# Performance work log

Hardware: AMD Instinct MI355X
Metric: run time of the kernel (lower is better)

## Reference

```python
import jax, jax.numpy as jnp
import numpy as np

N, E, B = 50000, 800000, 128
NF, ED, HID, HEADS, DH, OUT, L = 7, 2, 128, 4, 32, 64, 3
EPS = 1e-5
NEG_SLOPE = 0.2


def _layer_norm(x, g, b):
    mu = jnp.mean(x, axis=-1, keepdims=True)
    v = jnp.mean((x - mu) ** 2, axis=-1, keepdims=True)
    return g * (x - mu) / jnp.sqrt(v + EPS) + b


def setup_inputs() -> dict:
    key = jax.random.key(0)
    ks = jax.random.split(key, 32)
    s = 0.05
    inp = {
        "x": jax.random.normal(ks[0], (N, NF), jnp.float32),
        "edge_index": jax.random.randint(ks[1], (2, E), 0, N, jnp.int32),
        "edge_attr": jax.random.uniform(ks[2], (E, ED), jnp.float32),
        "batch": jnp.sort(jax.random.randint(ks[3], (N,), 0, B, jnp.int32)),
        # node encoder
        "enc_W": jax.random.normal(ks[4], (NF, HID)) * (1.0 / np.sqrt(NF)),
        "enc_b": jnp.zeros((HID,)),
        "enc_g": jnp.ones((HID,)),
        "enc_bb": jnp.zeros((HID,)),
        # GATv2 layers (stacked over L)
        "gat_Wsrc": jax.random.normal(ks[5], (L, HID, HID)) * (1.0 / np.sqrt(HID)),
        "gat_Wdst": jax.random.normal(ks[6], (L, HID, HID)) * (1.0 / np.sqrt(HID)),
        "gat_We": jax.random.normal(ks[7], (L, ED, HID)) * (1.0 / np.sqrt(ED)),
        "gat_att": jax.random.normal(ks[8], (L, HEADS, DH)) * s,
        "gat_bias": jnp.zeros((L, HID)),
        # GraphNorm per layer
        "gn_w": jnp.ones((L, HID)),
        "gn_b": jnp.zeros((L, HID)),
        "gn_s": jnp.ones((L, HID)),  # mean_scale
        # attention pooling
        "pool_W1": jax.random.normal(ks[9], (HID, HID)) * (1.0 / np.sqrt(HID)),
        "pool_b1": jnp.zeros((HID,)),
        "pool_W2": jax.random.normal(ks[10], (HID, 1)) * (1.0 / np.sqrt(HID)),
        # output mapper
        "map_W1": jax.random.normal(ks[11], (HID, HID)) * (1.0 / np.sqrt(HID)),
        "map_b1": jnp.zeros((HID,)),
        "map_g": jnp.ones((HID,)),
        "map_bb": jnp.zeros((HID,)),
        "map_W2": jax.random.normal(ks[12], (HID, OUT)) * (1.0 / np.sqrt(HID)),
        "map_b2": jnp.zeros((OUT,)),
    }
    return inp


def _segment_softmax(scores, seg, num_seg):
    # scores: [E2, HEADS], seg: [E2] destination node ids
    m = jax.ops.segment_max(scores, seg, num_segments=num_seg)
    ex = jnp.exp(scores - m[seg])
    denom = jax.ops.segment_sum(ex, seg, num_segments=num_seg)
    return ex / denom[seg]


def _gatv2(x, src, dst, ea, Wsrc, Wdst, We, att, bias):
    e2 = src.shape[0]
    xl = (x @ Wsrc)[src].reshape(e2, HEADS, DH)   # lin_l(x_j), source
    xr = (x @ Wdst)[dst].reshape(e2, HEADS, DH)   # lin_r(x_i), target
    ee = (ea @ We).reshape(e2, HEADS, DH)
    z = jax.nn.leaky_relu(xl + xr + ee, NEG_SLOPE)
    score = jnp.einsum("ehd,hd->eh", z, att)
    alpha = _segment_softmax(score, dst, N)       # softmax over incoming edges
    msg = (xl * alpha[:, :, None]).reshape(e2, HID)
    out = jax.ops.segment_sum(msg, dst, num_segments=N)
    return out + bias


def _graph_norm(x, batch, w, b, scale):
    cnt = jax.ops.segment_sum(jnp.ones((N,), x.dtype), batch, num_segments=B)
    cnt = jnp.maximum(cnt, 1.0)[:, None]
    mean = jax.ops.segment_sum(x, batch, num_segments=B) / cnt
    xc = x - scale * mean[batch]
    var = jax.ops.segment_sum(xc * xc, batch, num_segments=B) / cnt
    return w * xc / jnp.sqrt(var[batch] + EPS) + b


def reference(x, edge_index, edge_attr, batch, enc_W, enc_b, enc_g, enc_bb,
              gat_Wsrc, gat_Wdst, gat_We, gat_att, gat_bias, gn_w, gn_b, gn_s,
              pool_W1, pool_b1, pool_W2, map_W1, map_b1, map_g, map_bb,
              map_W2, map_b2):
    # node encoder: Linear -> ReLU -> LayerNorm
    h = _layer_norm(jax.nn.relu(x @ enc_W + enc_b), enc_g, enc_bb)

    # add self loops; self-loop edge_attr = mean of edge_attr (PyG fill_value='mean')
    loop = jnp.arange(N, dtype=edge_index.dtype)
    src = jnp.concatenate([edge_index[0], loop])
    dst = jnp.concatenate([edge_index[1], loop])
    ea_mean = jnp.mean(edge_attr, axis=0)
    ea = jnp.concatenate([edge_attr, jnp.broadcast_to(ea_mean, (N, ED))], axis=0)

    for i in range(L):
        out = _gatv2(h, src, dst, ea, gat_Wsrc[i], gat_Wdst[i], gat_We[i],
                     gat_att[i], gat_bias[i])
        out = out + h  # residual (in_dim == out_dim -> Identity proj)
        out = _graph_norm(out, batch, gn_w[i], gn_b[i], gn_s[i])
        h = jax.nn.elu(out)

    node_emb = h
    # attention pooling: softmax over ALL nodes (dim=0, as in source)
    scores = jnp.tanh(h @ pool_W1 + pool_b1) @ pool_W2          # [N, 1]
    weights = jax.nn.softmax(scores, axis=0)
    g = jax.ops.segment_sum(h * weights, batch, num_segments=B)  # [B, HID]

    # output mapper (dropout inactive at eval)
    g = _layer_norm(jax.nn.relu(g @ map_W1 + map_b1), map_g, map_bb)
    graph_emb = g @ map_W2 + map_b2
    return graph_emb, node_emb
```

## Files before the change

kernel.cpp:

```cpp
#include <hip/hip_runtime.h>
#include <hip/hip_bf16.h>

typedef __hip_bfloat16 bf16;
typedef __attribute__((ext_vector_type(8))) short short8;
typedef __attribute__((ext_vector_type(4))) float float4v;

#define Nn   50000
#define Ee   800000
#define E2   850000
#define Bb   128
#define NFd  7
#define HID  128
#define OUTD 64
#define EPS  1e-5f
#define SLOPE 0.2f
#define NSTRIP 3125
#define NPAIR  1563

#define MFMA16(a,b,c) __builtin_amdgcn_mfma_f32_16x16x32_bf16(a,b,c,0,0,0)

__device__ __forceinline__ float lane_bcast(float v, int l){
  return __int_as_float(__builtin_amdgcn_readlane(__float_as_int(v), l));
}
__device__ __forceinline__ float wred_sum(float v){
  #pragma unroll
  for (int o=32;o;o>>=1) v += __shfl_xor(v, o, 64);
  return v;
}
__device__ __forceinline__ float gred16_sum(float v){
  v += __shfl_xor(v,1,64); v += __shfl_xor(v,2,64);
  v += __shfl_xor(v,4,64); v += __shfl_xor(v,8,64);
  return v;
}
__device__ __forceinline__ unsigned fkey(float f){
  unsigned u = __float_as_uint(f);
  return (u & 0x80000000u) ? ~u : (u | 0x80000000u);
}
__device__ __forceinline__ float fkeyinv(unsigned k){
  unsigned u = (k & 0x80000000u) ? (k ^ 0x80000000u) : ~k;
  return __uint_as_float(u);
}
__device__ __forceinline__ float tanh_fast(float x){
  float e = __expf(fminf(fmaxf(2.f*x, -30.f), 30.f));
  return (e-1.f)/(e+1.f);
}
__device__ __forceinline__ float bf_lo(unsigned u){ return __uint_as_float(u<<16); }
__device__ __forceinline__ float bf_hi(unsigned u){ return __uint_as_float(u & 0xffff0000u); }
__device__ __forceinline__ unsigned short f2bs(float f){
  bf16 h = __float2bfloat16(f);
  return *reinterpret_cast<unsigned short*>(&h);
}
__device__ __forceinline__ unsigned pack2(float a, float b){
  return (unsigned)f2bs(a) | ((unsigned)f2bs(b) << 16);
}

__global__ __launch_bounds__(256) void k_encoder(
    const float* __restrict__ x, const float* __restrict__ W, const float* __restrict__ b,
    const float* __restrict__ g, const float* __restrict__ bbv,
    float* __restrict__ h, unsigned* __restrict__ hbu){
  int wv = (blockIdx.x*blockDim.x + threadIdx.x) >> 6;
  if (wv >= Nn) return;
  int lane = threadIdx.x & 63;
  int d0 = 2*lane, d1 = d0+1;
  float y0 = b[d0], y1 = b[d1];
  #pragma unroll
  for (int i=0;i<NFd;++i){
    float xv = x[wv*NFd + i];
    y0 = fmaf(xv, W[i*HID + d0], y0);
    y1 = fmaf(xv, W[i*HID + d1], y1);
  }
  y0 = fmaxf(y0, 0.f); y1 = fmaxf(y1, 0.f);
  float mu = wred_sum(y0+y1) * (1.f/HID);
  float c0 = y0-mu, c1 = y1-mu;
  float var = wred_sum(c0*c0 + c1*c1) * (1.f/HID);
  float rs = rsqrtf(var + EPS);
  float v0 = g[d0]*c0*rs + bbv[d0];
  float v1 = g[d1]*c1*rs + bbv[d1];
  *(float2*)(h + (size_t)wv*HID + d0) = make_float2(v0, v1);
  hbu[(size_t)wv*64 + lane] = pack2(v0, v1);
}

__global__ void k_ea_mean(const float* __restrict__ ea, float* __restrict__ eam){
  int tid = blockIdx.x*blockDim.x + threadIdx.x;
  const float2* ea2 = (const float2*)ea;
  float a0=0.f, a1=0.f;
  for (int e=tid; e<Ee; e += gridDim.x*blockDim.x){
    float2 v = ea2[e];
    a0 += v.x; a1 += v.y;
  }
  a0 = wred_sum(a0); a1 = wred_sum(a1);
  if ((threadIdx.x & 63)==0){
    atomicAdd(&eam[0], a0*(1.f/Ee));
    atomicAdd(&eam[1], a1*(1.f/Ee));
  }
}

__global__ void k_deg(const int* __restrict__ ei, int* __restrict__ deg){
  int e = blockIdx.x*blockDim.x + threadIdx.x;
  if (e >= E2) return;
  int d = (e < Ee) ? ei[Ee + e] : (e - Ee);
  atomicAdd(&deg[d], 1);
}

__global__ __launch_bounds__(1024) void k_scan(const int* __restrict__ deg,
    int* __restrict__ offs, int* __restrict__ cursor){
  __shared__ int wsum[16];
  __shared__ int tot_s;
  __shared__ int carry_s;
  int t = threadIdx.x, lane = t & 63, wid = t >> 6;
  if (t==0) carry_s = 0;
  __syncthreads();
  for (int base=0; base<Nn; base += 1024){
    int i = base + t;
    int v = (i < Nn) ? deg[i] : 0;
    int x = v;
    #pragma unroll
    for (int o=1;o<64;o<<=1){ int u = __shfl_up(x, o, 64); if (lane >= o) x += u; }
    if (lane==63) wsum[wid] = x;
    __syncthreads();
    if (t==0){ int s=0; for (int k=0;k<16;++k){ int tv=wsum[k]; wsum[k]=s; s+=tv; } tot_s = s; }
    __syncthreads();
    int excl = carry_s + wsum[wid] + x - v;
    if (i < Nn){ offs[i] = excl; cursor[i] = excl; }
    __syncthreads();
    if (t==0) carry_s += tot_s;
    __syncthreads();
  }
  if (t==0) offs[Nn] = carry_s;
}

__global__ void k_scatter(const int* __restrict__ ei, const float* __restrict__ ea,
    const float* __restrict__ eam, int* __restrict__ cursor,
    int* __restrict__ csrc, float2* __restrict__ cea){
  int e = blockIdx.x*blockDim.x + threadIdx.x;
  if (e >= E2) return;
  int s, d; float a0, a1;
  if (e < Ee){
    s = ei[e]; d = ei[Ee + e];
    float2 v = ((const float2*)ea)[e];
    a0 = v.x; a1 = v.y;
  } else {
    s = d = e - Ee; a0 = eam[0]; a1 = eam[1];
  }
  int pos = atomicAdd(&cursor[d], 1);
  csrc[pos] = s;
  cea[pos] = make_float2(a0, a1);
}

__global__ void k_gstart(const int* __restrict__ batch, int* __restrict__ gstart){
  int n = blockIdx.x*blockDim.x + threadIdx.x;
  if (n >= Nn) return;
  int bc = batch[n];
  int bp = (n==0) ? -1 : batch[n-1];
  for (int b = bp+1; b <= bc; ++b) gstart[b] = n;
  if (n == Nn-1){ for (int b = bc+1; b <= Bb; ++b) gstart[b] = Nn; }
}

__global__ __launch_bounds__(256) void k_dualgemm(
    const unsigned* __restrict__ hbu,
    const float* __restrict__ Wsrc, const float* __restrict__ Wdst,
    unsigned* __restrict__ hsb, float* __restrict__ hd){
  __shared__ unsigned short wt[256*HID];
  #pragma unroll
  for (int iter=0; iter<64; ++iter){
    int idx = iter*256 + threadIdx.x;
    int n = idx & 255, kp = idx >> 8;
    const float* Wp = (n < 128) ? Wsrc : (Wdst - 128);
    float w0 = Wp[(2*kp)*HID + n];
    float w1 = Wp[(2*kp+1)*HID + n];
    int byt = (n*256 + kp*4) ^ ((n&7)<<4);
    *(unsigned*)((char*)wt + byt) = pack2(w0, w1);
  }
  __syncthreads();
  int wid = threadIdx.x >> 6, lane = threadIdx.x & 63;
  int q = lane >> 4, c = lane & 15;
  const unsigned short* hb = (const unsigned short*)hbu;
  for (int pr = blockIdx.x*4 + wid; pr < NPAIR; pr += gridDim.x*4){
    int p0 = 2*pr, p1 = 2*pr + 1;
    bool v1 = (p1 < NSTRIP);
    int node0 = p0*16 + c;
    int node1 = v1 ? (p1*16 + c) : node0;
    short8 bf0[4], bf1[4];
    const unsigned short* hp0 = hb + (size_t)node0*HID + q*8;
    const unsigned short* hp1 = hb + (size_t)node1*HID + q*8;
    #pragma unroll
    for (int s=0;s<4;++s){
      bf0[s] = *(const short8*)(hp0 + s*32);
      bf1[s] = *(const short8*)(hp1 + s*32);
    }
    #pragma unroll 4
    for (int t=0;t<16;++t){
      float4v ac0 = {0.f,0.f,0.f,0.f}, ac1 = {0.f,0.f,0.f,0.f};
      #pragma unroll
      for (int s=0;s<4;++s){
        int row = t*16 + c;
        int byt = (row*256 + s*64 + q*16) ^ ((row&7)<<4);
        short8 af = *(const short8*)((const char*)wt + byt);
        ac0 = MFMA16(af, bf0[s], ac0);
        ac1 = MFMA16(af, bf1[s], ac1);
      }
      if (t < 8){
        int co = t*8 + q*2;
        *(uint2*)(hsb + (size_t)node0*64 + co) =
            make_uint2(pack2(ac0[0],ac0[1]), pack2(ac0[2],ac0[3]));
        if (v1) *(uint2*)(hsb + (size_t)node1*64 + co) =
            make_uint2(pack2(ac1[0],ac1[1]), pack2(ac1[2],ac1[3]));
      } else {
        int dd = (t-8)*16 + q*4;
        *(float4*)(hd + (size_t)node0*HID + dd) = make_float4(ac0[0],ac0[1],ac0[2],ac0[3]);
        if (v1) *(float4*)(hd + (size_t)node1*HID + dd) = make_float4(ac1[0],ac1[1],ac1[2],ac1[3]);
      }
    }
  }
}

__global__ __launch_bounds__(256) void k_edge(const unsigned* __restrict__ hsb,
    float* __restrict__ hdio, const float* __restrict__ h,
    const int* __restrict__ csrc, const float2* __restrict__ cea,
    const int* __restrict__ offs, const float* __restrict__ We,
    const float* __restrict__ att, const float* __restrict__ bias){
  int n = (blockIdx.x*blockDim.x + threadIdx.x) >> 6;
  if (n >= Nn) return;
  int lane = threadIdx.x & 63;
  int d0 = 2*lane, d1 = d0+1;
  float we00 = We[d0],       we01 = We[d1];
  float we10 = We[HID+d0],   we11 = We[HID+d1];
  float at0  = att[(lane>>4)*32 + (d0&31)];
  float at1  = att[(lane>>4)*32 + (d1&31)];
  float2 xr = *(const float2*)(hdio + (size_t)n*HID + d0);
  int e0 = offs[n], e1 = offs[n+1];
  float m = -1e30f, ssum = 0.f, acc0 = 0.f, acc1 = 0.f;
  int s_next = csrc[e0];
  float2 ea_next = cea[e0];
  for (int e = e0; e < e1; ++e){
    int s = s_next; float2 eav = ea_next;
    if (e+1 < e1){ s_next = csrc[e+1]; ea_next = cea[e+1]; }
    unsigned xlu = hsb[(size_t)s*64 + lane];
    float xl0 = bf_lo(xlu), xl1 = bf_hi(xlu);
    float z0 = fmaf(eav.y, we10, fmaf(eav.x, we00, xl0 + xr.x));
    float z1 = fmaf(eav.y, we11, fmaf(eav.x, we01, xl1 + xr.y));
    z0 = fmaxf(z0, SLOPE*z0);
    z1 = fmaxf(z1, SLOPE*z1);
    float sc = gred16_sum(fmaf(z1, at1, z0*at0));
    float nm = fmaxf(m, sc);
    float f  = __expf(m - nm);
    float p  = __expf(sc - nm);
    ssum = ssum*f + p;
    acc0 = fmaf(p, xl0, acc0*f);
    acc1 = fmaf(p, xl1, acc1*f);
    m = nm;
  }
  float inv = 1.f/ssum;
  float o0 = acc0*inv + bias[d0] + h[(size_t)n*HID + d0];
  float o1 = acc1*inv + bias[d1] + h[(size_t)n*HID + d1];
  *(float2*)(hdio + (size_t)n*HID + d0) = make_float2(o0, o1);
}

__global__ __launch_bounds__(128) void k_gn_reduce(const float* __restrict__ out,
    const int* __restrict__ gstart, float* __restrict__ gsum_, float* __restrict__ gsq_){
  int b = blockIdx.x >> 4, sub = blockIdx.x & 15;
  int ns = gstart[b], ne = gstart[b+1];
  int d = threadIdx.x;
  float s = 0.f, qq = 0.f;
  for (int n = ns + sub; n < ne; n += 16){
    float v = out[(size_t)n*HID + d];
    s += v; qq = fmaf(v, v, qq);
  }
  atomicAdd(&gsum_[b*HID + d], s);
  atomicAdd(&gsq_[b*HID + d], qq);
}

__global__ __launch_bounds__(256) void k_gn_apply(const float* __restrict__ out,
    const float* __restrict__ gsum_, const float* __restrict__ gsq_,
    const int* __restrict__ gstart, const int* __restrict__ batch,
    const float* __restrict__ gw, const float* __restrict__ gb,
    const float* __restrict__ gs, float* __restrict__ h,
    unsigned* __restrict__ hbu, float* __restrict__ emb){
  int n = (blockIdx.x*blockDim.x + threadIdx.x) >> 6;
  if (n >= Nn) return;
  int lane = threadIdx.x & 63;
  int b = batch[n];
  float icnt = 1.f / fmaxf((float)(gstart[b+1]-gstart[b]), 1.f);
  int d0 = 2*lane, d1 = d0+1;
  float2 x = *(const float2*)(out + (size_t)n*HID + d0);
  float mean0 = gsum_[b*HID+d0]*icnt, mean1 = gsum_[b*HID+d1]*icnt;
  float ms0 = mean0*gs[d0], ms1 = mean1*gs[d1];
  float var0 = gsq_[b*HID+d0]*icnt - ms0*(2.f*mean0 - ms0);
  float var1 = gsq_[b*HID+d1]*icnt - ms1*(2.f*mean1 - ms1);
  float rs0 = rsqrtf(fmaxf(var0, 0.f) + EPS);
  float rs1 = rsqrtf(fmaxf(var1, 0.f) + EPS);
  float y0 = gw[d0]*(x.x - ms0)*rs0 + gb[d0];
  float y1 = gw[d1]*(x.y - ms1)*rs1 + gb[d1];
  y0 = (y0 > 0.f) ? y0 : (__expf(y0) - 1.f);
  y1 = (y1 > 0.f) ? y1 : (__expf(y1) - 1.f);
  *(float2*)(h + (size_t)n*HID + d0) = make_float2(y0, y1);
  hbu[(size_t)n*64 + lane] = pack2(y0, y1);
  if (emb) *(float2*)(emb + (size_t)n*HID + d0) = make_float2(y0, y1);
}

__global__ __launch_bounds__(256) void k_pool_score(
    const unsigned* __restrict__ hbu,
    const float* __restrict__ W1, const float* __restrict__ b1, const float* __restrict__ W2,
    float* __restrict__ score, unsigned* __restrict__ mkey){
  __shared__ unsigned short wt[HID*HID];
  __shared__ float b1l[HID], w2l[HID];
  #pragma unroll
  for (int iter=0; iter<32; ++iter){
    int idx = iter*256 + threadIdx.x;
    int n = idx & 127, kp = idx >> 7;
    float w0 = W1[(2*kp)*HID + n];
    float w1 = W1[(2*kp+1)*HID + n];
    int byt = (n*256 + kp*4) ^ ((n&7)<<4);
    *(unsigned*)((char*)wt + byt) = pack2(w0, w1);
  }
  if (threadIdx.x < HID){ b1l[threadIdx.x] = b1[threadIdx.x]; w2l[threadIdx.x] = W2[threadIdx.x]; }
  __syncthreads();
  int wid = threadIdx.x >> 6, lane = threadIdx.x & 63;
  int q = lane >> 4, c = lane & 15;
  const unsigned short* hb = (const unsigned short*)hbu;
  float bmax = -1e30f;
  for (int p = blockIdx.x*4 + wid; p < NSTRIP; p += gridDim.x*4){
    int node = p*16 + c;
    short8 bf[4];
    const unsigned short* hp = hb + (size_t)node*HID + q*8;
    #pragma unroll
    for (int s=0;s<4;++s) bf[s] = *(const short8*)(hp + s*32);
    float part = 0.f;
    #pragma unroll
    for (int t=0;t<8;++t){
      float4v ac = {0.f,0.f,0.f,0.f};
      #pragma unroll
      for (int s=0;s<4;++s){
        int row = t*16 + c;
        int byt = (row*256 + s*64 + q*16) ^ ((row&7)<<4);
        ac = MFMA16(*(const short8*)((const char*)wt + byt), bf[s], ac);
      }
      int dim = t*16 + q*4;
      #pragma unroll
      for (int r=0;r<4;++r)
        part += tanh_fast(ac[r] + b1l[dim+r]) * w2l[dim+r];
    }
    part += __shfl_xor(part, 16, 64);
    part += __shfl_xor(part, 32, 64);
    if (q==0) score[node] = part;
    bmax = fmaxf(bmax, part);
  }
  #pragma unroll
  for (int o=32;o;o>>=1) bmax = fmaxf(bmax, __shfl_xor(bmax, o, 64));
  if (lane==0) atomicMax(mkey, fkey(bmax));
}

__global__ __launch_bounds__(128) void k_pool_reduce(const float* __restrict__ h,
    const float* __restrict__ score, const unsigned* __restrict__ mkey,
    const int* __restrict__ gstart, float* __restrict__ gsum, float* __restrict__ total){
  int b = blockIdx.x >> 4, sub = blockIdx.x & 15;
  int ns = gstart[b], ne = gstart[b+1];
  float mx = fkeyinv(*mkey);
  int d = threadIdx.x;
  float acc = 0.f, es = 0.f;
  for (int n = ns + sub; n < ne; n += 16){
    float ev = __expf(score[n] - mx);
    acc = fmaf(ev, h[(size_t)n*HID + d], acc);
    if (d==0) es += ev;
  }
  atomicAdd(&gsum[b*HID + d], acc);
  if (d==0) atomicAdd(total, es);
}

__global__ __launch_bounds__(64) void k_mapper(const float* __restrict__ gsum,
    const float* __restrict__ total,
    const float* __restrict__ W1, const float* __restrict__ b1,
    const float* __restrict__ g,  const float* __restrict__ bbv,
    const float* __restrict__ W2, const float* __restrict__ b2v,
    float* __restrict__ out0){
  int b = blockIdx.x, lane = threadIdx.x;
  float inv = 1.f/(*total);
  int d0 = 2*lane, d1 = d0+1;
  float gv0 = gsum[b*HID + d0]*inv, gv1 = gsum[b*HID + d1]*inv;
  float a0 = b1[d0], a1 = b1[d1];
  for (int i=0;i<HID;++i){
    float hv = lane_bcast((i&1) ? gv1 : gv0, i>>1);
    a0 = fmaf(hv, W1[i*HID + d0], a0);
    a1 = fmaf(hv, W1[i*HID + d1], a1);
  }
  a0 = fmaxf(a0, 0.f); a1 = fmaxf(a1, 0.f);
  float mu = wred_sum(a0+a1) * (1.f/HID);
  float c0 = a0-mu, c1 = a1-mu;
  float var = wred_sum(c0*c0 + c1*c1) * (1.f/HID);
  float rs = rsqrtf(var + EPS);
  float l0 = g[d0]*c0*rs + bbv[d0];
  float l1 = g[d1]*c1*rs + bbv[d1];
  float acc = b2v[lane];
  for (int j=0;j<HID;++j){
    float lv = lane_bcast((j&1) ? l1 : l0, j>>1);
    acc = fmaf(lv, W2[j*OUTD + lane], acc);
  }
  out0[b*OUTD + lane] = acc;
}

extern "C" void kernel_launch(void* const* d_in, const int* in_sizes, int n_in,
                              void* d_out, int out_size, void* d_ws, size_t ws_size,
                              hipStream_t stream){
  const float* x     = (const float*)d_in[0];
  const int*   ei    = (const int*)  d_in[1];
  const float* ea    = (const float*)d_in[2];
  const int*   batch = (const int*)  d_in[3];
  const float* encW  = (const float*)d_in[4];
  const float* encb  = (const float*)d_in[5];
  const float* encg  = (const float*)d_in[6];
  const float* encbb = (const float*)d_in[7];
  const float* gWsrc = (const float*)d_in[8];
  const float* gWdst = (const float*)d_in[9];
  const float* gWe   = (const float*)d_in[10];
  const float* gatt  = (const float*)d_in[11];
  const float* gbias = (const float*)d_in[12];
  const float* gnw   = (const float*)d_in[13];
  const float* gnb   = (const float*)d_in[14];
  const float* gns   = (const float*)d_in[15];
  const float* pW1   = (const float*)d_in[16];
  const float* pb1   = (const float*)d_in[17];
  const float* pW2   = (const float*)d_in[18];
  const float* mW1   = (const float*)d_in[19];
  const float* mb1   = (const float*)d_in[20];
  const float* mg    = (const float*)d_in[21];
  const float* mbb   = (const float*)d_in[22];
  const float* mW2   = (const float*)d_in[23];
  const float* mb2   = (const float*)d_in[24];

  char* w = (char*)d_ws;
  size_t off = 0;
  auto alloc = [&](size_t bytes)->char*{
    char* p = w + off;
    off += (bytes + 255) & ~(size_t)255;
    return p;
  };
  float*    h      = (float*)   alloc((size_t)Nn*HID*4);
  unsigned* hbu    = (unsigned*)alloc((size_t)Nn*64*4);
  unsigned* hsb    = (unsigned*)alloc((size_t)Nn*64*4);
  float*    hd     = (float*)   alloc((size_t)Nn*HID*4);
  int*      csrc   = (int*)     alloc((size_t)E2*4);
  float2*   cea    = (float2*)  alloc((size_t)E2*8);
  int*      offs   = (int*)     alloc((size_t)(Nn+1)*4);
  int*      cursor = (int*)     alloc((size_t)Nn*4);
  int*      deg    = (int*)     alloc((size_t)Nn*4);
  int*      gstart = (int*)     alloc((size_t)(Bb+1)*4);
  float*    score  = (float*)   alloc((size_t)Nn*4);
  float*    gsum   = (float*)   alloc((size_t)Bb*HID*4);
  float*    gnsum  = (float*)   alloc((size_t)Bb*HID*4*2);
  float*    scal   = (float*)   alloc(256);
  float*    eam   = scal;
  float*    total = scal + 2;
  unsigned* mkey  = (unsigned*)(scal + 3);
  float*    gnsq  = gnsum + Bb*HID;

  float* out_graph = (float*)d_out;
  float* out_node  = (float*)d_out + (size_t)Bb*OUTD;

  hipMemsetAsync(deg,  0, (size_t)Nn*4, stream);
  hipMemsetAsync(scal, 0, 256, stream);
  hipMemsetAsync(gsum, 0, (size_t)Bb*HID*4, stream);

  k_encoder<<<Nn/4, 256, 0, stream>>>(x, encW, encb, encg, encbb, h, hbu);
  k_ea_mean<<<256, 256, 0, stream>>>(ea, eam);
  k_deg<<<(E2+255)/256, 256, 0, stream>>>(ei, deg);
  k_scan<<<1, 1024, 0, stream>>>(deg, offs, cursor);
  k_scatter<<<(E2+255)/256, 256, 0, stream>>>(ei, ea, eam, cursor, csrc, cea);
  k_gstart<<<(Nn+255)/256, 256, 0, stream>>>(batch, gstart);

  for (int l = 0; l < 3; ++l){
    k_dualgemm<<<256, 256, 0, stream>>>(hbu, gWsrc + (size_t)l*HID*HID,
                                        gWdst + (size_t)l*HID*HID, hsb, hd);
    k_edge<<<Nn/4, 256, 0, stream>>>(hsb, hd, h, csrc, cea, offs,
                                     gWe + (size_t)l*2*HID,
                                     gatt + (size_t)l*4*32,
                                     gbias + (size_t)l*HID);
    hipMemsetAsync(gnsum, 0, (size_t)Bb*HID*4*2, stream);
    k_gn_reduce<<<Bb*16, 128, 0, stream>>>(hd, gstart, gnsum, gnsq);
    k_gn_apply<<<Nn/4, 256, 0, stream>>>(hd, gnsum, gnsq, gstart, batch,
                                         gnw + (size_t)l*HID, gnb + (size_t)l*HID,
                                         gns + (size_t)l*HID, h, hbu,
                                         (l==2) ? out_node : (float*)nullptr);
  }

  k_pool_score<<<256, 256, 0, stream>>>(hbu, pW1, pb1, pW2, score, mkey);
  k_pool_reduce<<<Bb*16, 128, 0, stream>>>(h, score, mkey, gstart, gsum, total);
  k_mapper<<<Bb, 64, 0, stream>>>(gsum, total, mW1, mb1, mg, mbb, mW2, mb2, out_graph);
}
```

Measured before the change: 671.4 us.

## Unroll GATv2 edge loop by two with prefetched gathers and lazy rescale

```diff
diff --git a/kernel.cpp b/kernel.cpp
--- a/kernel.cpp
+++ b/kernel.cpp
@@ -52,6 +52,11 @@
 }
 __device__ __forceinline__ unsigned pack2(float a, float b){
   return (unsigned)f2bs(a) | ((unsigned)f2bs(b) << 16);
+}
+__device__ __forceinline__ int xcd_swizzle(int bid, int nwg){
+  int q = nwg >> 3, r = nwg & 7;
+  int x = bid & 7, i = bid >> 3;
+  return (x < r ? x*(q+1) : r*(q+1) + (x-r)*q) + i;
 }
 
 __global__ __launch_bounds__(256) void k_encoder(
@@ -219,7 +224,8 @@
     const int* __restrict__ csrc, const float2* __restrict__ cea,
     const int* __restrict__ offs, const float* __restrict__ We,
     const float* __restrict__ att, const float* __restrict__ bias){
-  int n = (blockIdx.x*blockDim.x + threadIdx.x) >> 6;
+  int bid = xcd_swizzle(blockIdx.x, gridDim.x);
+  int n = (bid*256 + (int)threadIdx.x) >> 6;
   if (n >= Nn) return;
   int lane = threadIdx.x & 63;
   int d0 = 2*lane, d1 = d0+1;
@@ -230,25 +236,73 @@
   float2 xr = *(const float2*)(hdio + (size_t)n*HID + d0);
   int e0 = offs[n], e1 = offs[n+1];
   float m = -1e30f, ssum = 0.f, acc0 = 0.f, acc1 = 0.f;
-  int s_next = csrc[e0];
-  float2 ea_next = cea[e0];
-  for (int e = e0; e < e1; ++e){
-    int s = s_next; float2 eav = ea_next;
-    if (e+1 < e1){ s_next = csrc[e+1]; ea_next = cea[e+1]; }
-    unsigned xlu = hsb[(size_t)s*64 + lane];
-    float xl0 = bf_lo(xlu), xl1 = bf_hi(xlu);
-    float z0 = fmaf(eav.y, we10, fmaf(eav.x, we00, xl0 + xr.x));
-    float z1 = fmaf(eav.y, we11, fmaf(eav.x, we01, xl1 + xr.y));
-    z0 = fmaxf(z0, SLOPE*z0);
-    z1 = fmaxf(z1, SLOPE*z1);
+
+  int e = e0;
+  int npair = (e1 - e0) >> 1;
+  int sA, sB; float2 eA, eB; unsigned xA, xB;
+  if (npair > 0){
+    sA = csrc[e]; sB = csrc[e+1];
+    eA = cea[e];  eB = cea[e+1];
+    xA = hsb[(size_t)sA*64 + lane];
+    xB = hsb[(size_t)sB*64 + lane];
+  }
+  for (int i = 0; i < npair; ++i){
+    int sA_n=0, sB_n=0; float2 eA_n, eB_n; unsigned xA_n=0, xB_n=0;
+    if (i+1 < npair){
+      int en = e + 2;
+      sA_n = csrc[en]; sB_n = csrc[en+1];
+      eA_n = cea[en];  eB_n = cea[en+1];
+      xA_n = hsb[(size_t)sA_n*64 + lane];
+      xB_n = hsb[(size_t)sB_n*64 + lane];
+    }
+    float xA0 = bf_lo(xA), xA1 = bf_hi(xA);
+    float xB0 = bf_lo(xB), xB1 = bf_hi(xB);
+    float zA0 = fmaf(eA.y, we10, fmaf(eA.x, we00, xA0 + xr.x));
+    float zA1 = fmaf(eA.y, we11, fmaf(eA.x, we01, xA1 + xr.y));
+    float zB0 = fmaf(eB.y, we10, fmaf(eB.x, we00, xB0 + xr.x));
+    float zB1 = fmaf(eB.y, we11, fmaf(eB.x, we01, xB1 + xr.y));
+    zA0 = fmaxf(zA0, SLOPE*zA0); zA1 = fmaxf(zA1, SLOPE*zA1);
+    zB0 = fmaxf(zB0, SLOPE*zB0); zB1 = fmaxf(zB1, SLOPE*zB1);
+    float scA = gred16_sum(fmaf(zA1, at1, zA0*at0));
+    float scB = gred16_sum(fmaf(zB1, at1, zB0*at0));
+    float mAB = fmaxf(scA, scB);
+    float nm = fmaxf(m, mAB);
+    float pA = __expf(scA - nm);
+    float pB = __expf(scB - nm);
+    if (__any(mAB > m)){
+      float f = __expf(m - nm);
+      ssum = fmaf(ssum, f, pA + pB);
+      acc0 = fmaf(acc0, f, fmaf(pA, xA0, pB*xB0));
+      acc1 = fmaf(acc1, f, fmaf(pA, xA1, pB*xB1));
+      m = nm;
+    } else {
+      ssum += pA + pB;
+      acc0 = fmaf(pB, xB0, fmaf(pA, xA0, acc0));
+      acc1 = fmaf(pB, xB1, fmaf(pA, xA1, acc1));
+    }
+    e += 2;
+    sA=sA_n; sB=sB_n; eA=eA_n; eB=eB_n; xA=xA_n; xB=xB_n;
+  }
+  if (e < e1){
+    int s = csrc[e]; float2 eav = cea[e];
+    unsigned xu = hsb[(size_t)s*64 + lane];
+    float x0 = bf_lo(xu), x1 = bf_hi(xu);
+    float z0 = fmaf(eav.y, we10, fmaf(eav.x, we00, x0 + xr.x));
+    float z1 = fmaf(eav.y, we11, fmaf(eav.x, we01, x1 + xr.y));
+    z0 = fmaxf(z0, SLOPE*z0); z1 = fmaxf(z1, SLOPE*z1);
     float sc = gred16_sum(fmaf(z1, at1, z0*at0));
     float nm = fmaxf(m, sc);
-    float f  = __expf(m - nm);
-    float p  = __expf(sc - nm);
-    ssum = ssum*f + p;
-    acc0 = fmaf(p, xl0, acc0*f);
-    acc1 = fmaf(p, xl1, acc1*f);
-    m = nm;
+    float p = __expf(sc - nm);
+    if (__any(sc > m)){
+      float f = __expf(m - nm);
+      ssum = fmaf(ssum, f, p);
+      acc0 = fmaf(acc0, f, p*x0);
+      acc1 = fmaf(acc1, f, p*x1);
+    } else {
+      ssum += p;
+      acc0 = fmaf(p, x0, acc0);
+      acc1 = fmaf(p, x1, acc1);
+    }
   }
   float inv = 1.f/ssum;
   float o0 = acc0*inv + bias[d0] + h[(size_t)n*HID + d0];
```

Result: faster. 637.8 us (-5.0%).
